# Performance work log

Measured on AMD Instinct MI355X. Metric: run time of the kernel, lower is better.

## Reference

```python
import jax, jax.numpy as jnp
import numpy as np

EPS = 0.01  # Normalizer eps
N_NODES = 100000
N_EDGES = 1600000


def gcn_conv(x, edge_index, W, b, n_nodes):
    """PyG-style GCNConv: x @ W, symmetric-normalized aggregation with self-loops, + bias."""
    src = jnp.concatenate([edge_index[0], jnp.arange(n_nodes)])  # [E+N]
    dst = jnp.concatenate([edge_index[1], jnp.arange(n_nodes)])  # [E+N]
    h = x @ W  # [N, out]
    ones = jnp.ones_like(dst, dtype=h.dtype)
    deg = jax.ops.segment_sum(ones, dst, num_segments=n_nodes)  # [N]
    dinv = jnp.where(deg > 0, jax.lax.rsqrt(deg), 0.0)
    norm = dinv[src] * dinv[dst]  # [E+N]
    msgs = h[src] * norm[:, None]  # [E+N, out]  (largest intermediate)
    out = jax.ops.segment_sum(msgs, dst, num_segments=n_nodes)  # [N, out]
    return out + b


def setup_inputs() -> dict:
    key = jax.random.key(0)
    k = jax.random.split(key, 6)
    x = jax.random.normal(k[0], (N_NODES, 16), dtype=jnp.float32)
    edge_index = jax.random.randint(k[1], (2, N_EDGES), 0, N_NODES)
    W1 = jax.random.normal(k[2], (16, 64), dtype=jnp.float32) * 0.25
    b1 = jax.random.normal(k[3], (64,), dtype=jnp.float32) * 0.1
    W3 = jax.random.normal(k[4], (64, 32), dtype=jnp.float32) * 0.125
    b3 = jax.random.normal(k[5], (32,), dtype=jnp.float32) * 0.1
    return {"x": x, "edge_index": edge_index, "W1": W1, "b1": b1, "W3": W3, "b3": b3}


def reference(x, edge_index, W1, b1, W3, b3):
    n = x.shape[0]
    h = jax.nn.relu(gcn_conv(x, edge_index, W1, b1, n))
    h = jax.nn.relu(gcn_conv(h, edge_index, W3, b3, n))
    # Normalizer: sequential Welford observe over all nodes then normalize with
    # FINAL stats == population mean / clamped population variance.
    mean = h.mean(axis=0)  # [32]
    var = jnp.maximum(((h - mean) ** 2).mean(axis=0), EPS)  # [32]
    return (h - mean) * jax.lax.rsqrt(var)
```

## Files before the change

kernel.cpp:

```cpp
#include <hip/hip_runtime.h>
#include <hip/hip_fp16.h>

#define EPS 0.01f
#define SCAN_BS 512
#define NCHUNKS 256
#define BUCKET_SHIFT 9
#define BUCKET_SZ (1 << BUCKET_SHIFT)


__global__ __launch_bounds__(SCAN_BS) void k_scan_block(const int* __restrict__ in,
                                                        int* __restrict__ out,
                                                        int* __restrict__ bsum, int n) {
    __shared__ int sd[SCAN_BS];
    int t = threadIdx.x;
    int gid = blockIdx.x * SCAN_BS + t;
    int v = (gid < n) ? in[gid] : 0;
    sd[t] = v;
    __syncthreads();
    for (int off = 1; off < SCAN_BS; off <<= 1) {
        int x = (t >= off) ? sd[t - off] : 0;
        __syncthreads();
        sd[t] += x;
        __syncthreads();
    }
    if (gid < n) out[gid] = sd[t] - v;
    if (t == SCAN_BS - 1) bsum[blockIdx.x] = sd[t];
}

__global__ __launch_bounds__(SCAN_BS) void k_scan_tops(int* __restrict__ bsum, int nb) {
    __shared__ int sd[SCAN_BS];
    int t = threadIdx.x;
    int v = (t < nb) ? bsum[t] : 0;
    sd[t] = v;
    __syncthreads();
    for (int off = 1; off < SCAN_BS; off <<= 1) {
        int x = (t >= off) ? sd[t - off] : 0;
        __syncthreads();
        sd[t] += x;
        __syncthreads();
    }
    if (t < nb) bsum[t] = sd[t] - v;
}

__global__ __launch_bounds__(SCAN_BS) void k_scan_add(int* __restrict__ out,
                                                      const int* __restrict__ bsum, int n) {
    int gid = blockIdx.x * SCAN_BS + threadIdx.x;
    if (gid < n) out[gid] += bsum[blockIdx.x];
}


__global__ __launch_bounds__(256) void kA_bucket_hist(const int* __restrict__ dst,
                                                      int* __restrict__ bh, int e,
                                                      int nbuck, int ce) {
    extern __shared__ int hist[];
    int b = blockIdx.x, t = threadIdx.x;
    for (int i = t; i < nbuck; i += 256) hist[i] = 0;
    __syncthreads();
    int lo = b * ce, hi = min(lo + ce, e);
    for (int i = lo + t; i < hi; i += 256) atomicAdd(&hist[dst[i] >> BUCKET_SHIFT], 1);
    __syncthreads();
    for (int i = t; i < nbuck; i += 256) bh[i * NCHUNKS + b] = hist[i];
}

__global__ __launch_bounds__(256) void kC_bucket_scatter(const int* __restrict__ src,
                                                         const int* __restrict__ dst,
                                                         const int* __restrict__ bhs,
                                                         unsigned int* __restrict__ eb, int e,
                                                         int nbuck, int ce) {
    extern __shared__ int cur[];
    int b = blockIdx.x, t = threadIdx.x;
    for (int i = t; i < nbuck; i += 256) cur[i] = bhs[i * NCHUNKS + b];
    __syncthreads();
    int lo = b * ce, hi = min(lo + ce, e);
    for (int i = lo + t; i < hi; i += 256) {
        int s = src[i], d = dst[i];
        int pos = atomicAdd(&cur[d >> BUCKET_SHIFT], 1);
        eb[pos] = ((unsigned int)(d & (BUCKET_SZ - 1)) << 23) | (unsigned int)s;
    }
}

__global__ __launch_bounds__(256) void kDeg_scan_prescale(const unsigned int* __restrict__ eb,
                                                          const int* __restrict__ bhs,
                                                          const float* __restrict__ x,
                                                          int* __restrict__ degi,
                                                          float* __restrict__ dinv,
                                                          int* __restrict__ rowstart,
                                                          __half* __restrict__ xs,
                                                          float* __restrict__ partial,
                                                          int n, int nbuck, int e) {
    __shared__ int hist[BUCKET_SZ];
    __shared__ int ps[256];
    __shared__ float dv[BUCKET_SZ];
    int k = blockIdx.x, t = threadIdx.x;
    if (k == 0 && t < 64) partial[t] = 0.f;
    for (int i = t; i < BUCKET_SZ; i += 256) hist[i] = 0;
    __syncthreads();
    int lo = bhs[k * NCHUNKS];
    int hi = (k + 1 < nbuck) ? bhs[(k + 1) * NCHUNKS] : e;
    for (int i = lo + t; i < hi; i += 256) atomicAdd(&hist[eb[i] >> 23], 1);
    __syncthreads();
    int a0 = hist[2 * t], a1 = hist[2 * t + 1];
    ps[t] = a0 + a1;
    __syncthreads();
    for (int off = 1; off < 256; off <<= 1) {
        int v = (t >= off) ? ps[t - off] : 0;
        __syncthreads();
        ps[t] += v;
        __syncthreads();
    }
    int excl = ps[t] - (a0 + a1);
    int node0 = k << BUCKET_SHIFT;
    {
        int nd0 = node0 + 2 * t, nd1 = nd0 + 1;
        float d0 = rsqrtf((float)a0 + 1.0f);
        float d1 = rsqrtf((float)a1 + 1.0f);
        dv[2 * t] = d0;
        dv[2 * t + 1] = d1;
        if (nd0 < n) {
            degi[nd0] = a0;
            dinv[nd0] = d0;
            rowstart[nd0] = lo + excl;
        }
        if (nd1 < n) {
            degi[nd1] = a1;
            dinv[nd1] = d1;
            rowstart[nd1] = lo + excl + a0;
        }
    }
    __syncthreads();
    for (int i = t; i < BUCKET_SZ * 16; i += 256) {
        int rl = i >> 4;
        int node = node0 + rl;
        if (node < n) xs[(size_t)node * 16 + (i & 15)] = __float2half(x[(size_t)node * 16 + (i & 15)] * dv[rl]);
    }
}

__global__ __launch_bounds__(256) void kD_fill(const unsigned int* __restrict__ eb,
                                               const int* __restrict__ bhs,
                                               const int* __restrict__ rowstart,
                                               int* __restrict__ csr_src,
                                               int n, int nbuck, int e) {
    __shared__ int cur[BUCKET_SZ];
    int k = blockIdx.x, t = threadIdx.x;
    int node0 = k << BUCKET_SHIFT;
    for (int i = t; i < BUCKET_SZ; i += 256) {
        int node = node0 + i;
        cur[i] = (node < n) ? rowstart[node] : 0;
    }
    __syncthreads();
    int lo = bhs[k * NCHUNKS];
    int hi = (k + 1 < nbuck) ? bhs[(k + 1) * NCHUNKS] : e;
    for (int i = lo + t; i < hi; i += 256) {
        unsigned int p = eb[i];
        int dl = (int)(p >> 23);
        int s = (int)(p & 0x7fffffu);
        int pos = atomicAdd(&cur[dl], 1);
        csr_src[pos] = s;
    }
}


__global__ __launch_bounds__(256) void k_l1_fused(const int* __restrict__ rowstart,
                                                  const int* __restrict__ degi,
                                                  const int* __restrict__ csr_src,
                                                  const float* __restrict__ dinv,
                                                  const __half* __restrict__ xs,
                                                  const float* __restrict__ W1,
                                                  const float* __restrict__ b1,
                                                  const float* __restrict__ W3,
                                                  __half* __restrict__ h2s, int n) {
    __shared__ float w1[16 * 64];
    __shared__ float w3[64 * 32];
    __shared__ float bs[64];
    __shared__ __align__(16) float a[16 * 16];
    __shared__ float z[16 * 64];
    int t = threadIdx.x;
    for (int i = t; i < 16 * 64; i += 256) w1[i] = W1[i];
    for (int i = t; i < 64 * 32; i += 256) w3[i] = W3[i];
    if (t < 64) bs[t] = b1[t];

    int row0 = blockIdx.x * 16;
    int wv = t >> 6;
    int lane = t & 63;
    int c2 = lane & 7;
    int slot = lane >> 3;
    const __half2* xs2 = (const __half2*)xs;

    for (int nid = 0; nid < 4; ++nid) {
        int node = row0 + wv * 4 + nid;
        if (node < n) {
            const int* sp = csr_src + rowstart[node];
            int deg = degi[node];
            int L = (deg + 7) >> 3;
            int base = slot * L;
            int end = min(base + L, deg);
            float ax = 0.f, ay = 0.f, bx = 0.f, by = 0.f;
            int k = base;
            for (; k + 2 <= end; k += 2) {
                int s0 = sp[k], s1 = sp[k + 1];
                float2 v0 = __half22float2(xs2[(size_t)s0 * 8 + c2]);
                float2 v1 = __half22float2(xs2[(size_t)s1 * 8 + c2]);
                ax += v0.x; ay += v0.y;
                bx += v1.x; by += v1.y;
            }
            if (k < end) {
                int s0 = sp[k];
                float2 v0 = __half22float2(xs2[(size_t)s0 * 8 + c2]);
                ax += v0.x; ay += v0.y;
            }
            float sx = ax + bx, sy = ay + by;
            sx += __shfl_xor(sx, 8);  sy += __shfl_xor(sy, 8);
            sx += __shfl_xor(sx, 16); sy += __shfl_xor(sy, 16);
            sx += __shfl_xor(sx, 32); sy += __shfl_xor(sy, 32);
            if (slot == 0) {
                float2 self = __half22float2(xs2[(size_t)node * 8 + c2]);
                float dn = dinv[node];
                int r = wv * 4 + nid;
                ((float2*)(a + r * 16))[c2] = make_float2(dn * (sx + self.x), dn * (sy + self.y));
            }
        }
    }
    __syncthreads();

    for (int i = t; i < 1024; i += 256) {
        int r = i >> 6, c = i & 63;
        float acc = bs[c];
#pragma unroll
        for (int k = 0; k < 16; ++k) acc += a[r * 16 + k] * w1[k * 64 + c];
        z[i] = acc > 0.f ? acc : 0.f;
    }
    __syncthreads();
    for (int i = t; i < 512; i += 256) {
        int r = i >> 5, c = i & 31;
        float acc = 0.f;
#pragma unroll
        for (int k = 0; k < 64; ++k) acc += z[r * 64 + k] * w3[k * 32 + c];
        int row = row0 + r;
        if (row < n) h2s[(size_t)row * 32 + c] = __float2half(acc * dinv[row]);
    }
}


__global__ __launch_bounds__(256) void k_gather32_stats(const int* __restrict__ rowstart,
                                                        const int* __restrict__ degi,
                                                        const int* __restrict__ csr_src,
                                                        const float* __restrict__ dinv,
                                                        const __half* __restrict__ h2s,
                                                        const float* __restrict__ b3,
                                                        float* __restrict__ out,
                                                        float* __restrict__ partial, int n) {
    int t = threadIdx.x;
    int lane = t & 63;
    int c2 = lane & 15;
    int slot = lane >> 4;
    const __half2* h2 = (const __half2*)h2s;
    float2 bias = ((const float2*)b3)[c2];
    float s_x = 0.f, s_y = 0.f, q_x = 0.f, q_y = 0.f;
    for (int it = 0; it < 8; ++it) {
        int node = blockIdx.x * 32 + it * 4 + (t >> 6);
        if (node < n) {
            const int* sp = csr_src + rowstart[node];
            int deg = degi[node];
            int L = (deg + 3) >> 2;
            int base = slot * L;
            int end = min(base + L, deg);
            float ax = 0.f, ay = 0.f, bx = 0.f, by = 0.f;
            float cx = 0.f, cy = 0.f, dx = 0.f, dy = 0.f;
            int k = base;
            for (; k + 4 <= end; k += 4) {
                int s0 = sp[k], s1 = sp[k + 1], s2 = sp[k + 2], s3 = sp[k + 3];
                float2 v0 = __half22float2(h2[(size_t)s0 * 16 + c2]);
                float2 v1 = __half22float2(h2[(size_t)s1 * 16 + c2]);
                float2 v2 = __half22float2(h2[(size_t)s2 * 16 + c2]);
                float2 v3 = __half22float2(h2[(size_t)s3 * 16 + c2]);
                ax += v0.x; ay += v0.y;
                bx += v1.x; by += v1.y;
                cx += v2.x; cy += v2.y;
                dx += v3.x; dy += v3.y;
            }
            for (; k < end; ++k) {
                int s0 = sp[k];
                float2 v0 = __half22float2(h2[(size_t)s0 * 16 + c2]);
                ax += v0.x; ay += v0.y;
            }
            float sx = (ax + bx) + (cx + dx);
            float sy = (ay + by) + (cy + dy);
            sx += __shfl_xor(sx, 16); sy += __shfl_xor(sy, 16);
            sx += __shfl_xor(sx, 32); sy += __shfl_xor(sy, 32);
            if (slot == 0) {
                float2 self = __half22float2(h2[(size_t)node * 16 + c2]);
                float dn = dinv[node];
                float vx = dn * (sx + self.x) + bias.x;
                float vy = dn * (sy + self.y) + bias.y;
                vx = vx > 0.f ? vx : 0.f;
                vy = vy > 0.f ? vy : 0.f;
                ((float2*)(out + (size_t)node * 32))[c2] = make_float2(vx, vy);
                s_x += vx; s_y += vy;
                q_x += vx * vx; q_y += vy * vy;
            }
        }
    }
    __shared__ float ls[128], lq[128];
    int wv = t >> 6;
    if ((t & 63) < 16) {
        ls[wv * 32 + 2 * c2] = s_x;
        ls[wv * 32 + 2 * c2 + 1] = s_y;
        lq[wv * 32 + 2 * c2] = q_x;
        lq[wv * 32 + 2 * c2 + 1] = q_y;
    }
    __syncthreads();
    if (t < 32) {
        float a = 0.f, b = 0.f;
#pragma unroll
        for (int w = 0; w < 4; ++w) {
            a += ls[w * 32 + t];
            b += lq[w * 32 + t];
        }
        atomicAdd(&partial[t], a);
        atomicAdd(&partial[32 + t], b);
    }
}


__global__ void k_finalize(const float* __restrict__ partial, float* __restrict__ meaninv, int n) {
    int t = threadIdx.x;
    if (t < 32) {
        float invn = 1.0f / (float)n;
        float mean = partial[t] * invn;
        float var = partial[32 + t] * invn - mean * mean;
        var = var > EPS ? var : EPS;
        meaninv[t] = mean;
        meaninv[32 + t] = rsqrtf(var);
    }
}

__global__ void k_norm(float* __restrict__ h, const float* __restrict__ meaninv, int n) {
    long long idx = (long long)blockIdx.x * blockDim.x + threadIdx.x;
    if (idx < (long long)n * 32) {
        int c = (int)(idx & 31);
        h[idx] = (h[idx] - meaninv[c]) * meaninv[32 + c];
    }
}

extern "C" void kernel_launch(void* const* d_in, const int* in_sizes, int n_in,
                              void* d_out, int out_size, void* d_ws, size_t ws_size,
                              hipStream_t stream) {
    const float* x  = (const float*)d_in[0];
    const int* ei   = (const int*)d_in[1];
    const float* W1 = (const float*)d_in[2];
    const float* b1 = (const float*)d_in[3];
    const float* W3 = (const float*)d_in[4];
    const float* b3 = (const float*)d_in[5];

    const int N = in_sizes[0] / 16;
    const int E = in_sizes[1] / 2;
    const int* src = ei;
    const int* dst = ei + E;

    const int NBUCK = (N + BUCKET_SZ - 1) >> BUCKET_SHIFT;
    const int CE = (E + NCHUNKS - 1) / NCHUNKS;
    const int BH_TOTAL = NBUCK * NCHUNKS;

    char* ws = (char*)d_ws;
    int*   degi     = (int*)ws;          ws += (size_t)N * 4;
    float* dinv     = (float*)ws;        ws += (size_t)N * 4;
    int*   rowstart = (int*)ws;          ws += (size_t)N * 4;
    int*   bsum2    = (int*)ws;          ws += (size_t)SCAN_BS * 4;
    int*   bh       = (int*)ws;          ws += (size_t)BH_TOTAL * 4;
    int*   bhs      = (int*)ws;          ws += (size_t)BH_TOTAL * 4;
    unsigned int* eb = (unsigned int*)ws; ws += (size_t)E * 4;
    int*   csr_src  = (int*)ws;          ws += (size_t)E * 4;
    __half* xs      = (__half*)ws;       ws += (size_t)N * 16 * 2;
    __half* h2s     = (__half*)ws;       ws += (size_t)N * 32 * 2;
    float* partial  = (float*)ws;        ws += 64 * 4;
    float* meaninv  = (float*)ws;

    float* out = (float*)d_out;

    const int NB2 = (BH_TOTAL + SCAN_BS - 1) / SCAN_BS;

    kA_bucket_hist<<<NCHUNKS, 256, NBUCK * 4, stream>>>(dst, bh, E, NBUCK, CE);
    k_scan_block<<<NB2, SCAN_BS, 0, stream>>>(bh, bhs, bsum2, BH_TOTAL);
    k_scan_tops<<<1, SCAN_BS, 0, stream>>>(bsum2, NB2);
    k_scan_add<<<NB2, SCAN_BS, 0, stream>>>(bhs, bsum2, BH_TOTAL);
    kC_bucket_scatter<<<NCHUNKS, 256, NBUCK * 4, stream>>>(src, dst, bhs, eb, E, NBUCK, CE);

    kDeg_scan_prescale<<<NBUCK, 256, 0, stream>>>(eb, bhs, x, degi, dinv, rowstart, xs,
                                                  partial, N, NBUCK, E);
    kD_fill<<<NBUCK, 256, 0, stream>>>(eb, bhs, rowstart, csr_src, N, NBUCK, E);

    k_l1_fused<<<(N + 15) / 16, 256, 0, stream>>>(rowstart, degi, csr_src, dinv, xs,
                                                  W1, b1, W3, h2s, N);

    k_gather32_stats<<<(N + 31) / 32, 256, 0, stream>>>(rowstart, degi, csr_src, dinv, h2s,
                                                        b3, out, partial, N);

    k_finalize<<<1, 64, 0, stream>>>(partial, meaninv, N);
    k_norm<<<((long long)N * 32 + 255) / 256, 256, 0, stream>>>(out, meaninv, N);
}
```

Baseline: 194.6 us.

## Fuse CSR fill into degree kernel and split layer-2 gather into two column halves

The degree/prescale kernel now stages each bucket's packed edges in shared memory (up to 16K entries) and fills the CSR source array in place, so the separate fill kernel and its second global read of the bucket array go away. Layer-1 output is written as two separate 16-column half-precision arrays, and the layer-2 gather runs twice as many blocks, each gathering only one 32-byte half-row. Consecutive blocks are interleaved so that blocks working on the same half share a smaller working set. The large shared staging buffer (64KB) lowers occupancy of the fused kernel, and the split gather reads the CSR indices twice.

```diff
diff --git a/kernel.cpp b/kernel.cpp
--- a/kernel.cpp
+++ b/kernel.cpp
@@ -6,6 +6,7 @@
 #define NCHUNKS 256
 #define BUCKET_SHIFT 9
 #define BUCKET_SZ (1 << BUCKET_SHIFT)
+#define STAGE_CAP 16384
 
 
 __global__ __launch_bounds__(SCAN_BS) void k_scan_block(const int* __restrict__ in,
@@ -79,15 +80,17 @@
     }
 }
 
-__global__ __launch_bounds__(256) void kDeg_scan_prescale(const unsigned int* __restrict__ eb,
+__global__ __launch_bounds__(256) void kDeg_fill_prescale(const unsigned int* __restrict__ eb,
                                                           const int* __restrict__ bhs,
                                                           const float* __restrict__ x,
                                                           int* __restrict__ degi,
                                                           float* __restrict__ dinv,
                                                           int* __restrict__ rowstart,
+                                                          int* __restrict__ csr_src,
                                                           __half* __restrict__ xs,
                                                           float* __restrict__ partial,
                                                           int n, int nbuck, int e) {
+    __shared__ unsigned int ebs[STAGE_CAP];
     __shared__ int hist[BUCKET_SZ];
     __shared__ int ps[256];
     __shared__ float dv[BUCKET_SZ];
@@ -97,7 +100,13 @@
     __syncthreads();
     int lo = bhs[k * NCHUNKS];
     int hi = (k + 1 < nbuck) ? bhs[(k + 1) * NCHUNKS] : e;
-    for (int i = lo + t; i < hi; i += 256) atomicAdd(&hist[eb[i] >> 23], 1);
+    int cnt = hi - lo;
+    bool fits = (cnt <= STAGE_CAP);
+    for (int i = t; i < cnt; i += 256) {
+        unsigned int p = eb[lo + i];
+        if (fits) ebs[i] = p;
+        atomicAdd(&hist[p >> 23], 1);
+    }
     __syncthreads();
     int a0 = hist[2 * t], a1 = hist[2 * t + 1];
     ps[t] = a0 + a1;
@@ -110,6 +119,7 @@
     }
     int excl = ps[t] - (a0 + a1);
     int node0 = k << BUCKET_SHIFT;
+    int rs0 = lo + excl, rs1 = lo + excl + a0;
     {
         int nd0 = node0 + 2 * t, nd1 = nd0 + 1;
         float d0 = rsqrtf((float)a0 + 1.0f);
@@ -119,42 +129,29 @@
         if (nd0 < n) {
             degi[nd0] = a0;
             dinv[nd0] = d0;
-            rowstart[nd0] = lo + excl;
+            rowstart[nd0] = rs0;
         }
         if (nd1 < n) {
             degi[nd1] = a1;
             dinv[nd1] = d1;
-            rowstart[nd1] = lo + excl + a0;
-        }
-    }
-    __syncthreads();
+            rowstart[nd1] = rs1;
+        }
+    }
+    __syncthreads();
+    hist[2 * t] = rs0;
+    hist[2 * t + 1] = rs1;
     for (int i = t; i < BUCKET_SZ * 16; i += 256) {
         int rl = i >> 4;
         int node = node0 + rl;
-        if (node < n) xs[(size_t)node * 16 + (i & 15)] = __float2half(x[(size_t)node * 16 + (i & 15)] * dv[rl]);
-    }
-}
-
-__global__ __launch_bounds__(256) void kD_fill(const unsigned int* __restrict__ eb,
-                                               const int* __restrict__ bhs,
-                                               const int* __restrict__ rowstart,
-                                               int* __restrict__ csr_src,
-                                               int n, int nbuck, int e) {
-    __shared__ int cur[BUCKET_SZ];
-    int k = blockIdx.x, t = threadIdx.x;
-    int node0 = k << BUCKET_SHIFT;
-    for (int i = t; i < BUCKET_SZ; i += 256) {
-        int node = node0 + i;
-        cur[i] = (node < n) ? rowstart[node] : 0;
-    }
-    __syncthreads();
-    int lo = bhs[k * NCHUNKS];
-    int hi = (k + 1 < nbuck) ? bhs[(k + 1) * NCHUNKS] : e;
-    for (int i = lo + t; i < hi; i += 256) {
-        unsigned int p = eb[i];
+        if (node < n)
+            xs[(size_t)node * 16 + (i & 15)] = __float2half(x[(size_t)node * 16 + (i & 15)] * dv[rl]);
+    }
+    __syncthreads();
+    for (int i = t; i < cnt; i += 256) {
+        unsigned int p = fits ? ebs[i] : eb[lo + i];
         int dl = (int)(p >> 23);
         int s = (int)(p & 0x7fffffu);
-        int pos = atomicAdd(&cur[dl], 1);
+        int pos = atomicAdd(&hist[dl], 1);
         csr_src[pos] = s;
     }
 }
@@ -168,7 +165,8 @@
                                                   const float* __restrict__ W1,
                                                   const float* __restrict__ b1,
                                                   const float* __restrict__ W3,
-                                                  __half* __restrict__ h2s, int n) {
+                                                  __half* __restrict__ h2sA,
+                                                  __half* __restrict__ h2sB, int n) {
     __shared__ float w1[16 * 64];
     __shared__ float w3[64 * 32];
     __shared__ float bs[64];
@@ -236,88 +234,94 @@
 #pragma unroll
         for (int k = 0; k < 64; ++k) acc += z[r * 64 + k] * w3[k * 32 + c];
         int row = row0 + r;
-        if (row < n) h2s[(size_t)row * 32 + c] = __float2half(acc * dinv[row]);
-    }
-}
-
-
-__global__ __launch_bounds__(256) void k_gather32_stats(const int* __restrict__ rowstart,
-                                                        const int* __restrict__ degi,
-                                                        const int* __restrict__ csr_src,
-                                                        const float* __restrict__ dinv,
-                                                        const __half* __restrict__ h2s,
-                                                        const float* __restrict__ b3,
-                                                        float* __restrict__ out,
-                                                        float* __restrict__ partial, int n) {
+        if (row < n) {
+            __half hv = __float2half(acc * dinv[row]);
+            if (c < 16) h2sA[(size_t)row * 16 + c] = hv;
+            else        h2sB[(size_t)row * 16 + (c - 16)] = hv;
+        }
+    }
+}
+
+
+__global__ __launch_bounds__(256) void k_gather16x2_stats(const int* __restrict__ rowstart,
+                                                          const int* __restrict__ degi,
+                                                          const int* __restrict__ csr_src,
+                                                          const float* __restrict__ dinv,
+                                                          const __half* __restrict__ h2sA,
+                                                          const __half* __restrict__ h2sB,
+                                                          const float* __restrict__ b3,
+                                                          float* __restrict__ out,
+                                                          float* __restrict__ partial, int n) {
+    int g = blockIdx.x;
+    int half = (g >> 2) & 1;
+    int nblk = (g >> 3) * 4 + (g & 3);
+    int M = (n + 31) >> 5;
+    if (nblk >= M) return;
+    const __half2* h2 = (const __half2*)(half ? h2sB : h2sA);
+    int col0 = half << 4;
     int t = threadIdx.x;
     int lane = t & 63;
-    int c2 = lane & 15;
-    int slot = lane >> 4;
-    const __half2* h2 = (const __half2*)h2s;
-    float2 bias = ((const float2*)b3)[c2];
+    int c2 = lane & 7;
+    int slot = lane >> 3;
+    float2 bias = make_float2(b3[col0 + 2 * c2], b3[col0 + 2 * c2 + 1]);
     float s_x = 0.f, s_y = 0.f, q_x = 0.f, q_y = 0.f;
     for (int it = 0; it < 8; ++it) {
-        int node = blockIdx.x * 32 + it * 4 + (t >> 6);
+        int node = nblk * 32 + it * 4 + (t >> 6);
         if (node < n) {
             const int* sp = csr_src + rowstart[node];
             int deg = degi[node];
-            int L = (deg + 3) >> 2;
+            int L = (deg + 7) >> 3;
             int base = slot * L;
             int end = min(base + L, deg);
             float ax = 0.f, ay = 0.f, bx = 0.f, by = 0.f;
-            float cx = 0.f, cy = 0.f, dx = 0.f, dy = 0.f;
             int k = base;
-            for (; k + 4 <= end; k += 4) {
-                int s0 = sp[k], s1 = sp[k + 1], s2 = sp[k + 2], s3 = sp[k + 3];
-                float2 v0 = __half22float2(h2[(size_t)s0 * 16 + c2]);
-                float2 v1 = __half22float2(h2[(size_t)s1 * 16 + c2]);
-                float2 v2 = __half22float2(h2[(size_t)s2 * 16 + c2]);
-                float2 v3 = __half22float2(h2[(size_t)s3 * 16 + c2]);
+            for (; k + 2 <= end; k += 2) {
+                int s0 = sp[k], s1 = sp[k + 1];
+                float2 v0 = __half22float2(h2[(size_t)s0 * 8 + c2]);
+                float2 v1 = __half22float2(h2[(size_t)s1 * 8 + c2]);
                 ax += v0.x; ay += v0.y;
                 bx += v1.x; by += v1.y;
-                cx += v2.x; cy += v2.y;
-                dx += v3.x; dy += v3.y;
-            }
-            for (; k < end; ++k) {
+            }
+            if (k < end) {
                 int s0 = sp[k];
-                float2 v0 = __half22float2(h2[(size_t)s0 * 16 + c2]);
+                float2 v0 = __half22float2(h2[(size_t)s0 * 8 + c2]);
                 ax += v0.x; ay += v0.y;
             }
-            float sx = (ax + bx) + (cx + dx);
-            float sy = (ay + by) + (cy + dy);
+            float sx = ax + bx, sy = ay + by;
+            sx += __shfl_xor(sx, 8);  sy += __shfl_xor(sy, 8);
             sx += __shfl_xor(sx, 16); sy += __shfl_xor(sy, 16);
             sx += __shfl_xor(sx, 32); sy += __shfl_xor(sy, 32);
             if (slot == 0) {
-                float2 self = __half22float2(h2[(size_t)node * 16 + c2]);
+                float2 self = __half22float2(h2[(size_t)node * 8 + c2]);
                 float dn = dinv[node];
                 float vx = dn * (sx + self.x) + bias.x;
                 float vy = dn * (sy + self.y) + bias.y;
                 vx = vx > 0.f ? vx : 0.f;
                 vy = vy > 0.f ? vy : 0.f;
-                ((float2*)(out + (size_t)node * 32))[c2] = make_float2(vx, vy);
+                ((float2*)(out + (size_t)node * 32 + col0))[c2] = make_float2(vx, vy);
                 s_x += vx; s_y += vy;
                 q_x += vx * vx; q_y += vy * vy;
             }
         }
     }
-    __shared__ float ls[128], lq[128];
+    __shared__ float ls[64], lq[64];
     int wv = t >> 6;
-    if ((t & 63) < 16) {
-        ls[wv * 32 + 2 * c2] = s_x;
-        ls[wv * 32 + 2 * c2 + 1] = s_y;
-        lq[wv * 32 + 2 * c2] = q_x;
-        lq[wv * 32 + 2 * c2 + 1] = q_y;
-    }
-    __syncthreads();
-    if (t < 32) {
+    if (lane < 8) {
+        ls[wv * 16 + 2 * c2] = s_x;
+        ls[wv * 16 + 2 * c2 + 1] = s_y;
+        lq[wv * 16 + 2 * c2] = q_x;
+        lq[wv * 16 + 2 * c2 + 1] = q_y;
+    }
+    __syncthreads();
+    if (t < 16) {
         float a = 0.f, b = 0.f;
 #pragma unroll
         for (int w = 0; w < 4; ++w) {
-            a += ls[w * 32 + t];
-            b += lq[w * 32 + t];
-        }
-        atomicAdd(&partial[t], a);
-        atomicAdd(&partial[32 + t], b);
+            a += ls[w * 16 + t];
+            b += lq[w * 16 + t];
+        }
+        atomicAdd(&partial[col0 + t], a);
+        atomicAdd(&partial[32 + col0 + t], b);
     }
 }
 
@@ -371,7 +375,8 @@
     unsigned int* eb = (unsigned int*)ws; ws += (size_t)E * 4;
     int*   csr_src  = (int*)ws;          ws += (size_t)E * 4;
     __half* xs      = (__half*)ws;       ws += (size_t)N * 16 * 2;
-    __half* h2s     = (__half*)ws;       ws += (size_t)N * 32 * 2;
+    __half* h2sA    = (__half*)ws;       ws += (size_t)N * 16 * 2;
+    __half* h2sB    = (__half*)ws;       ws += (size_t)N * 16 * 2;
     float* partial  = (float*)ws;        ws += 64 * 4;
     float* meaninv  = (float*)ws;
 
@@ -385,15 +390,16 @@
     k_scan_add<<<NB2, SCAN_BS, 0, stream>>>(bhs, bsum2, BH_TOTAL);
     kC_bucket_scatter<<<NCHUNKS, 256, NBUCK * 4, stream>>>(src, dst, bhs, eb, E, NBUCK, CE);
 
-    kDeg_scan_prescale<<<NBUCK, 256, 0, stream>>>(eb, bhs, x, degi, dinv, rowstart, xs,
-                                                  partial, N, NBUCK, E);
-    kD_fill<<<NBUCK, 256, 0, stream>>>(eb, bhs, rowstart, csr_src, N, NBUCK, E);
+    kDeg_fill_prescale<<<NBUCK, 256, 0, stream>>>(eb, bhs, x, degi, dinv, rowstart,
+                                                  csr_src, xs, partial, N, NBUCK, E);
 
     k_l1_fused<<<(N + 15) / 16, 256, 0, stream>>>(rowstart, degi, csr_src, dinv, xs,
-                                                  W1, b1, W3, h2s, N);
-
-    k_gather32_stats<<<(N + 31) / 32, 256, 0, stream>>>(rowstart, degi, csr_src, dinv, h2s,
-                                                        b3, out, partial, N);
+                                                  W1, b1, W3, h2sA, h2sB, N);
+
+    const int M = (N + 31) >> 5;
+    const int G = ((M + 3) / 4) * 8;
+    k_gather16x2_stats<<<G, 256, 0, stream>>>(rowstart, degi, csr_src, dinv, h2sA, h2sB,
+                                              b3, out, partial, N);
 
     k_finalize<<<1, 64, 0, stream>>>(partial, meaninv, N);
     k_norm<<<((long long)N * 32 + 255) / 256, 256, 0, stream>>>(out, meaninv, N);
```

Result: no change. 192.4 us (-1.1%).

## Fuse CSR fill into degree/prescale kernel and merge finalize into norm

Applied to the files above, without the earlier changes.

Merges the CSR fill pass into the degree-histogram kernel, staging each bucket's edges in LDS (up to 16384 entries) so the bucket array is read from global memory once instead of twice. The per-node row starts are kept in shared memory, which removes the rowstart reload. The x prescale is vectorized to float2/half2. The finalize kernel is folded into k_norm, which recomputes the mean and inverse std per block and processes float4s. Together these remove two launches. The cost is 64KB of static LDS per block, which lowers occupancy, plus redundant stats computation in every norm block.

```diff
diff --git a/kernel.cpp b/kernel.cpp
--- a/kernel.cpp
+++ b/kernel.cpp
@@ -6,6 +6,7 @@
 #define NCHUNKS 256
 #define BUCKET_SHIFT 9
 #define BUCKET_SZ (1 << BUCKET_SHIFT)
+#define STAGE_CAP 16384
 
 
 __global__ __launch_bounds__(SCAN_BS) void k_scan_block(const int* __restrict__ in,
@@ -79,15 +80,17 @@
     }
 }
 
-__global__ __launch_bounds__(256) void kDeg_scan_prescale(const unsigned int* __restrict__ eb,
+__global__ __launch_bounds__(256) void kDeg_fill_prescale(const unsigned int* __restrict__ eb,
                                                           const int* __restrict__ bhs,
                                                           const float* __restrict__ x,
                                                           int* __restrict__ degi,
                                                           float* __restrict__ dinv,
                                                           int* __restrict__ rowstart,
+                                                          int* __restrict__ csr_src,
                                                           __half* __restrict__ xs,
                                                           float* __restrict__ partial,
                                                           int n, int nbuck, int e) {
+    __shared__ unsigned int ebs[STAGE_CAP];
     __shared__ int hist[BUCKET_SZ];
     __shared__ int ps[256];
     __shared__ float dv[BUCKET_SZ];
@@ -97,7 +100,13 @@
     __syncthreads();
     int lo = bhs[k * NCHUNKS];
     int hi = (k + 1 < nbuck) ? bhs[(k + 1) * NCHUNKS] : e;
-    for (int i = lo + t; i < hi; i += 256) atomicAdd(&hist[eb[i] >> 23], 1);
+    int cnt = hi - lo;
+    bool fits = (cnt <= STAGE_CAP);
+    for (int i = t; i < cnt; i += 256) {
+        unsigned int p = eb[lo + i];
+        if (fits) ebs[i] = p;
+        atomicAdd(&hist[p >> 23], 1);
+    }
     __syncthreads();
     int a0 = hist[2 * t], a1 = hist[2 * t + 1];
     ps[t] = a0 + a1;
@@ -110,6 +119,7 @@
     }
     int excl = ps[t] - (a0 + a1);
     int node0 = k << BUCKET_SHIFT;
+    int rs0 = lo + excl, rs1 = lo + excl + a0;
     {
         int nd0 = node0 + 2 * t, nd1 = nd0 + 1;
         float d0 = rsqrtf((float)a0 + 1.0f);
@@ -119,42 +129,36 @@
         if (nd0 < n) {
             degi[nd0] = a0;
             dinv[nd0] = d0;
-            rowstart[nd0] = lo + excl;
+            rowstart[nd0] = rs0;
         }
         if (nd1 < n) {
             degi[nd1] = a1;
             dinv[nd1] = d1;
-            rowstart[nd1] = lo + excl + a0;
-        }
-    }
-    __syncthreads();
-    for (int i = t; i < BUCKET_SZ * 16; i += 256) {
-        int rl = i >> 4;
-        int node = node0 + rl;
-        if (node < n) xs[(size_t)node * 16 + (i & 15)] = __float2half(x[(size_t)node * 16 + (i & 15)] * dv[rl]);
-    }
-}
-
-__global__ __launch_bounds__(256) void kD_fill(const unsigned int* __restrict__ eb,
-                                               const int* __restrict__ bhs,
-                                               const int* __restrict__ rowstart,
-                                               int* __restrict__ csr_src,
-                                               int n, int nbuck, int e) {
-    __shared__ int cur[BUCKET_SZ];
-    int k = blockIdx.x, t = threadIdx.x;
-    int node0 = k << BUCKET_SHIFT;
-    for (int i = t; i < BUCKET_SZ; i += 256) {
-        int node = node0 + i;
-        cur[i] = (node < n) ? rowstart[node] : 0;
-    }
-    __syncthreads();
-    int lo = bhs[k * NCHUNKS];
-    int hi = (k + 1 < nbuck) ? bhs[(k + 1) * NCHUNKS] : e;
-    for (int i = lo + t; i < hi; i += 256) {
-        unsigned int p = eb[i];
+            rowstart[nd1] = rs1;
+        }
+    }
+    __syncthreads();
+    hist[2 * t] = rs0;
+    hist[2 * t + 1] = rs1;
+    {
+        const float2* xf2 = (const float2*)x;
+        __half2* xs2 = (__half2*)xs;
+        for (int i = t; i < BUCKET_SZ * 8; i += 256) {
+            int rl = i >> 3;
+            int node = node0 + rl;
+            if (node < n) {
+                float2 vv = xf2[(size_t)node * 8 + (i & 7)];
+                float d = dv[rl];
+                xs2[(size_t)node * 8 + (i & 7)] = __floats2half2_rn(vv.x * d, vv.y * d);
+            }
+        }
+    }
+    __syncthreads();
+    for (int i = t; i < cnt; i += 256) {
+        unsigned int p = fits ? ebs[i] : eb[lo + i];
         int dl = (int)(p >> 23);
         int s = (int)(p & 0x7fffffu);
-        int pos = atomicAdd(&cur[dl], 1);
+        int pos = atomicAdd(&hist[dl], 1);
         csr_src[pos] = s;
     }
 }
@@ -322,23 +326,29 @@
 }
 
 
-__global__ void k_finalize(const float* __restrict__ partial, float* __restrict__ meaninv, int n) {
+__global__ void k_norm(float* __restrict__ h, const float* __restrict__ partial, int n) {
+    __shared__ __align__(16) float mv[64];
     int t = threadIdx.x;
     if (t < 32) {
         float invn = 1.0f / (float)n;
         float mean = partial[t] * invn;
         float var = partial[32 + t] * invn - mean * mean;
         var = var > EPS ? var : EPS;
-        meaninv[t] = mean;
-        meaninv[32 + t] = rsqrtf(var);
-    }
-}
-
-__global__ void k_norm(float* __restrict__ h, const float* __restrict__ meaninv, int n) {
-    long long idx = (long long)blockIdx.x * blockDim.x + threadIdx.x;
-    if (idx < (long long)n * 32) {
-        int c = (int)(idx & 31);
-        h[idx] = (h[idx] - meaninv[c]) * meaninv[32 + c];
+        mv[t] = mean;
+        mv[32 + t] = rsqrtf(var);
+    }
+    __syncthreads();
+    int idx = blockIdx.x * blockDim.x + threadIdx.x;
+    if (idx < n * 8) {
+        int c4 = idx & 7;
+        float4 v = ((float4*)h)[idx];
+        float4 m = ((const float4*)mv)[c4];
+        float4 iv = ((const float4*)(mv + 32))[c4];
+        v.x = (v.x - m.x) * iv.x;
+        v.y = (v.y - m.y) * iv.y;
+        v.z = (v.z - m.z) * iv.z;
+        v.w = (v.w - m.w) * iv.w;
+        ((float4*)h)[idx] = v;
     }
 }
 
@@ -373,7 +383,6 @@
     __half* xs      = (__half*)ws;       ws += (size_t)N * 16 * 2;
     __half* h2s     = (__half*)ws;       ws += (size_t)N * 32 * 2;
     float* partial  = (float*)ws;        ws += 64 * 4;
-    float* meaninv  = (float*)ws;
 
     float* out = (float*)d_out;
 
@@ -385,9 +394,8 @@
     k_scan_add<<<NB2, SCAN_BS, 0, stream>>>(bhs, bsum2, BH_TOTAL);
     kC_bucket_scatter<<<NCHUNKS, 256, NBUCK * 4, stream>>>(src, dst, bhs, eb, E, NBUCK, CE);
 
-    kDeg_scan_prescale<<<NBUCK, 256, 0, stream>>>(eb, bhs, x, degi, dinv, rowstart, xs,
-                                                  partial, N, NBUCK, E);
-    kD_fill<<<NBUCK, 256, 0, stream>>>(eb, bhs, rowstart, csr_src, N, NBUCK, E);
+    kDeg_fill_prescale<<<NBUCK, 256, 0, stream>>>(eb, bhs, x, degi, dinv, rowstart,
+                                                  csr_src, xs, partial, N, NBUCK, E);
 
     k_l1_fused<<<(N + 15) / 16, 256, 0, stream>>>(rowstart, degi, csr_src, dinv, xs,
                                                   W1, b1, W3, h2s, N);
@@ -395,6 +403,5 @@
     k_gather32_stats<<<(N + 31) / 32, 256, 0, stream>>>(rowstart, degi, csr_src, dinv, h2s,
                                                         b3, out, partial, N);
 
-    k_finalize<<<1, 64, 0, stream>>>(partial, meaninv, N);
-    k_norm<<<((long long)N * 32 + 255) / 256, 256, 0, stream>>>(out, meaninv, N);
-}
+    k_norm<<<(N * 8 + 255) / 256, 256, 0, stream>>>(out, partial, N);
+}
```

New measurement: 182.8 us. 6.0% less time.
